# Kernel tuning notes

Hardware: AMD Instinct MI355X
Metric: run time of the kernel (lower is better)

The kernel has to match this reference:

```python
import jax, jax.numpy as jnp
import numpy as np


def setup_inputs() -> dict:
    key = jax.random.key(0)
    ks = jax.random.split(key, 10)
    B, T = 256, 256
    num_q, dk, dv, C = 1000, 128, 128, 32
    xn_k = (2.0 / (dk + C)) ** 0.5   # xavier_normal for Mk
    xn_v = (2.0 / (C + dv)) ** 0.5   # xavier_normal for Mv
    return dict(
        skills=jax.random.randint(ks[0], (B, T), 0, num_q),
        responses=jax.random.randint(ks[1], (B, T), 0, 2),
        k_emb=jax.random.normal(ks[2], (num_q, dk), dtype=jnp.float32) * 0.05,
        v_emb=jax.random.normal(ks[3], (2 * num_q, dv), dtype=jnp.float32) * 0.05,
        Mk=jax.random.normal(ks[4], (dk, C), dtype=jnp.float32) * xn_k,
        Mv0=jax.random.normal(ks[5], (C, dv), dtype=jnp.float32) * xn_v,
        f_W=jax.random.normal(ks[6], (2 * dk, dk), dtype=jnp.float32) * 0.05,
        f_b=jnp.zeros((dk,), jnp.float32),
        p_W=jax.random.normal(ks[7], (dk, 1), dtype=jnp.float32) * 0.05,
        p_b=jnp.zeros((1,), jnp.float32),
        e_W=jax.random.normal(ks[8], (dv, dv), dtype=jnp.float32) * 0.05,
        e_b=jnp.zeros((dv,), jnp.float32),
        a_W=jax.random.normal(ks[9], (dv, dv), dtype=jnp.float32) * 0.05,
        a_b=jnp.zeros((dv,), jnp.float32),
    )


def reference(skills, responses, k_emb, v_emb, Mk, Mv0, f_W, f_b,
              p_W, p_b, e_W, e_b, a_W, a_b):
    num_q = k_emb.shape[0]
    B = skills.shape[0]
    masked_r = responses * (responses > -1).astype(responses.dtype)
    qr = skills + num_q * masked_r
    kt_all = k_emb[skills]   # (B, T, dk)
    vt_all = v_emb[qr]       # (B, T, dv)
    Mvt0 = jnp.broadcast_to(Mv0[None], (B,) + Mv0.shape)  # (B, C, dv)

    def step(Mvt, xs):
        kt, vt = xs                                      # (B,dk), (B,dv)
        wt = jax.nn.softmax(kt @ Mk, axis=-1)            # (B, C) read weights
        rt = jnp.einsum('bc,bcd->bd', wt, Mvt)           # memory read
        ft = jnp.tanh(jnp.concatenate([rt, kt], axis=-1) @ f_W + f_b)
        pt = jax.nn.sigmoid(ft @ p_W + p_b)[:, 0]        # (B,)
        et = jax.nn.sigmoid(vt @ e_W + e_b)              # erase gate
        at = jnp.tanh(vt @ a_W + a_b)                    # add vector
        Mvt = Mvt * (1.0 - wt[:, :, None] * et[:, None, :]) \
              + wt[:, :, None] * at[:, None, :]
        return Mvt, pt

    xs = (jnp.swapaxes(kt_all, 0, 1), jnp.swapaxes(vt_all, 0, 1))  # time-major
    _, p = jax.lax.scan(step, Mvt0, xs)                  # (T, B)
    p = jnp.swapaxes(p, 0, 1)                            # (B, T)
    pred = p[:, :-1]
    true = responses[:, 1:].astype(jnp.float32)
    return pred, true
```

## Files before the change

kernel.cpp:

```cpp
#include <hip/hip_runtime.h>
#include <math.h>

#define BB 256
#define TT 256
#define NQ 1000
#define DK 128
#define DV 128
#define CC 32

typedef short s16x8 __attribute__((ext_vector_type(8)));
typedef float f32x4 __attribute__((ext_vector_type(4)));
typedef float f32x2 __attribute__((ext_vector_type(2)));

__device__ __forceinline__ float fast_sigmoid(float x) {
    x = fminf(fmaxf(x, -30.f), 30.f);
    return 1.f / (1.f + __expf(-x));
}
__device__ __forceinline__ float fast_tanh(float x) {
    x = fminf(fmaxf(x, -15.f), 15.f);
    float t = __expf(2.f * x);
    return (t - 1.f) / (t + 1.f);
}
__device__ __forceinline__ unsigned short f2bf(float f) {
    unsigned u = __float_as_uint(f);
    u += 0x7fffu + ((u >> 16) & 1u);
    return (unsigned short)(u >> 16);
}
__device__ __forceinline__ float bf2f(unsigned short h) {
    return __uint_as_float((unsigned)h << 16);
}
__device__ __forceinline__ unsigned u4get(uint4 v, int i) {
    return i == 0 ? v.x : i == 1 ? v.y : i == 2 ? v.z : v.w;
}
__device__ __forceinline__ f32x2 mk2(float x, float y) { f32x2 r; r.x = x; r.y = y; return r; }
__device__ __forceinline__ f32x2 fma2(f32x2 a, f32x2 b, f32x2 c) {
    return __builtin_elementwise_fma(a, b, c);
}
__device__ __forceinline__ s16x8 cvt8(float4 v0, float4 v1) {
    s16x8 f;
    f[0] = (short)f2bf(v0.x); f[1] = (short)f2bf(v0.y);
    f[2] = (short)f2bf(v0.z); f[3] = (short)f2bf(v0.w);
    f[4] = (short)f2bf(v1.x); f[5] = (short)f2bf(v1.y);
    f[6] = (short)f2bf(v1.z); f[7] = (short)f2bf(v1.w);
    return f;
}

__global__ __launch_bounds__(256) void conv_kernel(
    const float* __restrict__ eW, const float* __restrict__ aW,
    const float* __restrict__ fW, const float* __restrict__ Mk,
    unsigned short* __restrict__ eWt, unsigned short* __restrict__ aWt,
    unsigned short* __restrict__ fWat, unsigned short* __restrict__ fWbt,
    unsigned short* __restrict__ Mkt)
{
    int idx = blockIdx.x * 256 + threadIdx.x;
    if (idx < 16384) {
        int n = idx >> 7, k = idx & 127;
        eWt[idx] = f2bf(eW[k * 128 + n]);
    } else if (idx < 32768) {
        int i = idx - 16384; int n = i >> 7, k = i & 127;
        aWt[i] = f2bf(aW[k * 128 + n]);
    } else if (idx < 49152) {
        int i = idx - 32768; int n = i >> 7, k = i & 127;
        fWat[i] = f2bf(fW[k * 128 + n]);
    } else if (idx < 65536) {
        int i = idx - 49152; int n = i >> 7, k = i & 127;
        fWbt[i] = f2bf(fW[(128 + k) * 128 + n]);
    } else if (idx < 69632) {
        int i = idx - 65536; int n = i >> 7, k = i & 127;
        Mkt[i] = f2bf(Mk[k * 32 + n]);
    }
}

__global__ __launch_bounds__(256) void pre_kernel(
    const int* __restrict__ skills, const int* __restrict__ responses,
    const float* __restrict__ k_emb, const float* __restrict__ v_emb,
    const float* __restrict__ fb, const float* __restrict__ eb,
    const float* __restrict__ ab,
    const unsigned short* __restrict__ Mkt, const unsigned short* __restrict__ fWbt,
    const unsigned short* __restrict__ eWt, const unsigned short* __restrict__ aWt,
    float* __restrict__ Wo, unsigned* __restrict__ EA,
    unsigned short* __restrict__ Ko, float* __restrict__ outTrue,
    int t0, int Tc)
{
    const int tid = threadIdx.x;
    const int lane = tid & 63;
    const int m_base = (tid >> 6) * 16;
    const int mrow = lane & 15, quad = lane >> 4;
    const size_t base = (size_t)blockIdx.x * 64;

    __shared__ __align__(16) unsigned short Wlds[128 * 136];

    int grow = (int)base + m_base + mrow;
    int gb = grow / Tc;
    int gt = t0 + (grow - gb * Tc);
    int gi = gb * TT + gt;
    int s = skills[gi];
    int r = responses[gi];
    int q = s + NQ * ((r > -1) ? r : 0);
    if (quad == 0 && gt >= 1) outTrue[gb * (TT - 1) + (gt - 1)] = (float)r;

    {
        int n = tid >> 3, k0 = (tid & 7) * 16;
        *(s16x8*)&Wlds[n * 136 + k0]     = *(const s16x8*)&Mkt[n * 128 + k0];
        *(s16x8*)&Wlds[n * 136 + k0 + 8] = *(const s16x8*)&Mkt[n * 128 + k0 + 8];
    }

    s16x8 aF[4];
    {
        const float* kr = k_emb + (size_t)s * DK + quad * 8;
#pragma unroll
        for (int kb = 0; kb < 4; ++kb)
            aF[kb] = cvt8(*(const float4*)(kr + kb * 32),
                          *(const float4*)(kr + kb * 32 + 4));
    }
    __syncthreads();

    {
        f32x4 l0 = {0.f, 0.f, 0.f, 0.f}, l1 = {0.f, 0.f, 0.f, 0.f};
#pragma unroll
        for (int kb = 0; kb < 4; ++kb) {
            s16x8 b0 = *(const s16x8*)&Wlds[mrow * 136 + kb * 32 + quad * 8];
            s16x8 b1 = *(const s16x8*)&Wlds[(16 + mrow) * 136 + kb * 32 + quad * 8];
            l0 = __builtin_amdgcn_mfma_f32_16x16x32_bf16(aF[kb], b0, l0, 0, 0, 0);
            l1 = __builtin_amdgcn_mfma_f32_16x16x32_bf16(aF[kb], b1, l1, 0, 0, 0);
        }
#pragma unroll
        for (int reg = 0; reg < 4; ++reg) {
            float a0 = l0[reg], a1 = l1[reg];
            float m = fmaxf(a0, a1);
#pragma unroll
            for (int off = 1; off < 16; off <<= 1)
                m = fmaxf(m, __shfl_xor(m, off, 64));
            float e0 = __expf(a0 - m), e1 = __expf(a1 - m);
            float ssum = e0 + e1;
#pragma unroll
            for (int off = 1; off < 16; off <<= 1)
                ssum += __shfl_xor(ssum, off, 64);
            float inv = 1.f / ssum;
            size_t rowg = base + m_base + quad * 4 + reg;
            Wo[rowg * 32 + mrow]      = e0 * inv;
            Wo[rowg * 32 + 16 + mrow] = e1 * inv;
        }
    }
    __syncthreads();

    {
        int n = tid >> 1, k0 = (tid & 1) * 64;
#pragma unroll
        for (int j = 0; j < 8; ++j)
            *(s16x8*)&Wlds[n * 136 + k0 + j * 8] = *(const s16x8*)&fWbt[n * 128 + k0 + j * 8];
    }
    __syncthreads();

    s16x8 vF[4];
    {
        const float* vr = v_emb + (size_t)q * DV + quad * 8;
#pragma unroll
        for (int kb = 0; kb < 4; ++kb)
            vF[kb] = cvt8(*(const float4*)(vr + kb * 32),
                          *(const float4*)(vr + kb * 32 + 4));
    }

#pragma unroll
    for (int nt = 0; nt < 8; ++nt) {
        f32x4 acc = {0.f, 0.f, 0.f, 0.f};
#pragma unroll
        for (int kb = 0; kb < 4; ++kb) {
            s16x8 bf = *(const s16x8*)&Wlds[(nt * 16 + mrow) * 136 + kb * 32 + quad * 8];
            acc = __builtin_amdgcn_mfma_f32_16x16x32_bf16(aF[kb], bf, acc, 0, 0, 0);
        }
        int col = nt * 16 + mrow;
        float fbv = fb[col];
#pragma unroll
        for (int reg = 0; reg < 4; ++reg) {
            size_t rr = base + m_base + quad * 4 + reg;
            Ko[rr * 128 + col] = f2bf(acc[reg] + fbv);
        }
    }
    __syncthreads();

    {
        int n = tid >> 1, k0 = (tid & 1) * 64;
#pragma unroll
        for (int j = 0; j < 8; ++j)
            *(s16x8*)&Wlds[n * 136 + k0 + j * 8] = *(const s16x8*)&eWt[n * 128 + k0 + j * 8];
    }
    __syncthreads();

    float etr[8][4];
#pragma unroll
    for (int nt = 0; nt < 8; ++nt) {
        f32x4 acc = {0.f, 0.f, 0.f, 0.f};
#pragma unroll
        for (int kb = 0; kb < 4; ++kb) {
            s16x8 bf = *(const s16x8*)&Wlds[(nt * 16 + mrow) * 136 + kb * 32 + quad * 8];
            acc = __builtin_amdgcn_mfma_f32_16x16x32_bf16(vF[kb], bf, acc, 0, 0, 0);
        }
        int col = nt * 16 + mrow;
        float ebv = eb[col];
#pragma unroll
        for (int reg = 0; reg < 4; ++reg)
            etr[nt][reg] = fast_sigmoid(acc[reg] + ebv);
    }
    __syncthreads();

    {
        int n = tid >> 1, k0 = (tid & 1) * 64;
#pragma unroll
        for (int j = 0; j < 8; ++j)
            *(s16x8*)&Wlds[n * 136 + k0 + j * 8] = *(const s16x8*)&aWt[n * 128 + k0 + j * 8];
    }
    __syncthreads();

#pragma unroll
    for (int nt = 0; nt < 8; ++nt) {
        f32x4 acc = {0.f, 0.f, 0.f, 0.f};
#pragma unroll
        for (int kb = 0; kb < 4; ++kb) {
            s16x8 bf = *(const s16x8*)&Wlds[(nt * 16 + mrow) * 136 + kb * 32 + quad * 8];
            acc = __builtin_amdgcn_mfma_f32_16x16x32_bf16(vF[kb], bf, acc, 0, 0, 0);
        }
        int col = nt * 16 + mrow;
        float abv = ab[col];
#pragma unroll
        for (int reg = 0; reg < 4; ++reg) {
            size_t rr = base + m_base + quad * 4 + reg;
            int bb = (int)(rr / (size_t)Tc);
            int t  = (int)(rr - (size_t)bb * Tc);
            size_t o4 = (((size_t)bb * (Tc >> 5) + (t >> 5)) * 8 + ((t >> 2) & 7)) * 128 + col;
            unsigned lo = f2bf(etr[nt][reg]);
            unsigned hi = (unsigned)f2bf(fast_tanh(acc[reg] + abv)) << 16;
            EA[o4 * 4 + (t & 3)] = hi | lo;
        }
    }
}


#define CH 32
#define WROW 36
#define RSTR 136
#define SB() __builtin_amdgcn_sched_barrier(0)

#define LOAD_W(gg) do {                                                       \
    const float* ws = Wb + (size_t)(gg) * CH * 32;                            \
    wr0 = *(const float4*)(ws + tid * 8);                                     \
    wr1 = *(const float4*)(ws + tid * 8 + 4);                                 \
} while (0)

#define PUB_W(gg) do {                                                        \
    float* wd = &Wl[(gg) & 1][lr * WROW + lq * 8];                            \
    *(float4*)wd = wr0; *(float4*)(wd + 4) = wr1;                             \
} while (0)

#define LOAD_EA(ER, gg) do {                                                  \
    const uint4* src = EA4 + ((size_t)(bq + (gg))) * 1024 + tid;              \
    _Pragma("unroll")                                                         \
    for (int j = 0; j < 8; ++j) ER[j] = src[j * 128];                         \
} while (0)

#define PREF8(A0,A1,A2,A3,A4,A5,A6,A7, rowidx) do {                           \
    const float* _wr = wlc + (rowidx) * WROW;                                 \
    A0 = *(const float4*)(_wr + 0);  A1 = *(const float4*)(_wr + 4);          \
    A2 = *(const float4*)(_wr + 8);  A3 = *(const float4*)(_wr + 12);         \
    A4 = *(const float4*)(_wr + 16); A5 = *(const float4*)(_wr + 20);         \
    A6 = *(const float4*)(_wr + 24); A7 = *(const float4*)(_wr + 28);         \
} while (0)

#define STEP8(A0,A1,A2,A3,A4,A5,A6,A7, ER, tl) do {                           \
    f32x2 w2[16];                                                             \
    w2[0]  = mk2(A0.x, A0.y); w2[1]  = mk2(A0.z, A0.w);                       \
    w2[2]  = mk2(A1.x, A1.y); w2[3]  = mk2(A1.z, A1.w);                       \
    w2[4]  = mk2(A2.x, A2.y); w2[5]  = mk2(A2.z, A2.w);                       \
    w2[6]  = mk2(A3.x, A3.y); w2[7]  = mk2(A3.z, A3.w);                       \
    w2[8]  = mk2(A4.x, A4.y); w2[9]  = mk2(A4.z, A4.w);                       \
    w2[10] = mk2(A5.x, A5.y); w2[11] = mk2(A5.z, A5.w);                       \
    w2[12] = mk2(A6.x, A6.y); w2[13] = mk2(A6.z, A6.w);                       \
    w2[14] = mk2(A7.x, A7.y); w2[15] = mk2(A7.z, A7.w);                       \
    unsigned ea = u4get(ER[(tl) >> 2], (tl) & 3);                             \
    float e = __uint_as_float(ea << 16);                                      \
    float a = __uint_as_float(ea & 0xffff0000u);                              \
    f32x2 ne2 = mk2(-e, -e);                                                  \
    f32x2 a2  = mk2(a, a);                                                    \
    f32x2 r0 = mk2(0.f, 0.f), r1 = r0, r2 = r0, r3 = r0;                      \
    _Pragma("unroll")                                                         \
    for (int q = 0; q < 4; ++q) {                                             \
        r0 = fma2(w2[4*q+0], Mv2[4*q+0], r0);                                 \
        r1 = fma2(w2[4*q+1], Mv2[4*q+1], r1);                                 \
        r2 = fma2(w2[4*q+2], Mv2[4*q+2], r2);                                 \
        r3 = fma2(w2[4*q+3], Mv2[4*q+3], r3);                                 \
    }                                                                         \
    f32x2 rs = (r0 + r1) + (r2 + r3);                                         \
    slp[(tl) * RSTR + tid] = f2bf(rs.x + rs.y);                               \
    _Pragma("unroll")                                                         \
    for (int i = 0; i < 16; ++i)                                              \
        Mv2[i] = fma2(w2[i], fma2(ne2, Mv2[i], a2), Mv2[i]);                  \
} while (0)

#define SEQ_CHUNK(ER, gg, SL) do {                                            \
    const float* wlc = Wl[(gg) & 1];                                          \
    unsigned short* slp = SL;                                                 \
    PREF8(w0,w1,w2_,w3_,w4_,w5_,w6_,w7_, 0);                                  \
    _Pragma("unroll")                                                         \
    for (int tp = 0; tp < 16; ++tp) {                                         \
        SB(); PREF8(u0,u1,u2,u3,u4,u5,u6,u7, 2 * tp + 1); SB();               \
        STEP8(w0,w1,w2_,w3_,w4_,w5_,w6_,w7_, ER, 2 * tp);                     \
        SB(); PREF8(w0,w1,w2_,w3_,w4_,w5_,w6_,w7_,                            \
                    (2 * tp + 2 < 32) ? (2 * tp + 2) : 31); SB();             \
        STEP8(u0,u1,u2,u3,u4,u5,u6,u7, ER, 2 * tp + 1);                       \
    }                                                                         \
} while (0)

__device__ __forceinline__ void consume_chunk(
    int gc, const unsigned short* sl, const unsigned short* fWl,
    int b, int Tc, int t0,
    const unsigned short* __restrict__ Ko, const float* __restrict__ pW,
    float pbv, float* __restrict__ pred, int tid)
{
    const int lane = tid & 63;
    const int cw = (tid >> 6) & 1;
    const int mrow = lane & 15, quad = lane >> 4;
    s16x8 aF[4];
#pragma unroll
    for (int kb = 0; kb < 4; ++kb)
        aF[kb] = *(const s16x8*)&sl[(cw * 16 + mrow) * RSTR + kb * 32 + quad * 8];
    float p0 = 0.f, p1 = 0.f, p2 = 0.f, p3 = 0.f;
    size_t rbase = (size_t)b * Tc + gc * CH + cw * 16 + quad * 4;
#pragma unroll
    for (int nt = 0; nt < 8; ++nt) {
        f32x4 acc = {0.f, 0.f, 0.f, 0.f};
#pragma unroll
        for (int kb = 0; kb < 4; ++kb) {
            s16x8 bf = *(const s16x8*)&fWl[(nt * 16 + mrow) * RSTR + kb * 32 + quad * 8];
            acc = __builtin_amdgcn_mfma_f32_16x16x32_bf16(aF[kb], bf, acc, 0, 0, 0);
        }
        int col = nt * 16 + mrow;
        float pw = pW[col];
        p0 = fmaf(fast_tanh(acc[0] + bf2f(Ko[(rbase + 0) * 128 + col])), pw, p0);
        p1 = fmaf(fast_tanh(acc[1] + bf2f(Ko[(rbase + 1) * 128 + col])), pw, p1);
        p2 = fmaf(fast_tanh(acc[2] + bf2f(Ko[(rbase + 2) * 128 + col])), pw, p2);
        p3 = fmaf(fast_tanh(acc[3] + bf2f(Ko[(rbase + 3) * 128 + col])), pw, p3);
    }
#pragma unroll
    for (int off = 1; off < 16; off <<= 1) {
        p0 += __shfl_xor(p0, off, 64); p1 += __shfl_xor(p1, off, 64);
        p2 += __shfl_xor(p2, off, 64); p3 += __shfl_xor(p3, off, 64);
    }
    if (mrow == 0) {
        int tb = t0 + gc * CH + cw * 16 + quad * 4;
        float ps[4] = {p0, p1, p2, p3};
#pragma unroll
        for (int reg = 0; reg < 4; ++reg) {
            int t = tb + reg;
            if (t < TT - 1) pred[b * (TT - 1) + t] = fast_sigmoid(ps[reg] + pbv);
        }
    }
}

__global__ __launch_bounds__(256, 1) void fused_kernel(
    const float* __restrict__ W, const unsigned* __restrict__ EA,
    const float* __restrict__ Mv0, const unsigned short* __restrict__ Ko,
    const unsigned short* __restrict__ fWat, const float* __restrict__ pW,
    const float* __restrict__ pb,
    float* __restrict__ pred, float* __restrict__ MvWS,
    int t0, int Tc, int doInit, int doSave)
{
    const int b = blockIdx.x;
    const int tid = threadIdx.x;
    const int nch = Tc / CH;

    __shared__ __align__(16) float Wl[2][CH * WROW];
    __shared__ __align__(16) unsigned short rtl[2][CH * RSTR];
    __shared__ __align__(16) unsigned short fWl[128 * RSTR];

    {
        int n = tid >> 1, k0 = (tid & 1) * 64;
#pragma unroll
        for (int j = 0; j < 8; ++j)
            *(s16x8*)&fWl[n * RSTR + k0 + j * 8] = *(const s16x8*)&fWat[n * 128 + k0 + j * 8];
    }

    const int lr = tid >> 2, lq = tid & 3;
    const float* __restrict__ Wb = W + (size_t)b * Tc * 32;
    const uint4* __restrict__ EA4 = (const uint4*)EA;
    const int bq = b * nch;
    f32x2 Mv2[16];
    float4 wr0, wr1;
    float4 w0, w1, w2_, w3_, w4_, w5_, w6_, w7_;
    float4 u0, u1, u2, u3, u4, u5, u6, u7;
    uint4 erA[8], erB[8];
    float pbv = 0.f;

    if (tid < 128) {
        if (doInit) {
#pragma unroll
            for (int i = 0; i < 16; ++i)
                Mv2[i] = mk2(Mv0[(2 * i) * 128 + tid], Mv0[(2 * i + 1) * 128 + tid]);
        } else {
#pragma unroll
            for (int i = 0; i < 16; ++i)
                Mv2[i] = mk2(MvWS[(size_t)b * 4096 + (2 * i) * 128 + tid],
                             MvWS[(size_t)b * 4096 + (2 * i + 1) * 128 + tid]);
        }
        LOAD_W(0); PUB_W(0);
        LOAD_EA(erA, 0);
        if (nch > 1) LOAD_W(1);
    } else {
        pbv = pb[0];
    }
    __syncthreads();

    for (int g = 0; g < nch; g += 2) {
        if (tid < 128) {
            if (g + 1 < nch) PUB_W(g + 1);
            if (g + 2 < nch) LOAD_W(g + 2);
            if (g + 1 < nch) LOAD_EA(erB, g + 1);
            SEQ_CHUNK(erA, g, rtl[0]);
        } else if (g >= 1) {
            consume_chunk(g - 1, rtl[1], fWl, b, Tc, t0, Ko, pW, pbv, pred, tid);
        }
        __syncthreads();

        if (tid < 128) {
            if (g + 1 < nch) {
                if (g + 2 < nch) PUB_W(g + 2);
                if (g + 3 < nch) LOAD_W(g + 3);
                if (g + 2 < nch) LOAD_EA(erA, g + 2);
                SEQ_CHUNK(erB, g + 1, rtl[1]);
            }
        } else {
            consume_chunk(g, rtl[0], fWl, b, Tc, t0, Ko, pW, pbv, pred, tid);
        }
        __syncthreads();
    }
    if (!(nch & 1) && tid >= 128) {
        consume_chunk(nch - 1, rtl[1], fWl, b, Tc, t0, Ko, pW, pbv, pred, tid);
    }

    if (doSave && tid < 128) {
#pragma unroll
        for (int i = 0; i < 16; ++i) {
            MvWS[(size_t)b * 4096 + (2 * i) * 128 + tid]     = Mv2[i].x;
            MvWS[(size_t)b * 4096 + (2 * i + 1) * 128 + tid] = Mv2[i].y;
        }
    }
}


extern "C" void kernel_launch(void* const* d_in, const int* in_sizes, int n_in,
                              void* d_out, int out_size, void* d_ws, size_t ws_size,
                              hipStream_t stream) {
    const int*   skills    = (const int*)d_in[0];
    const int*   responses = (const int*)d_in[1];
    const float* k_emb     = (const float*)d_in[2];
    const float* v_emb     = (const float*)d_in[3];
    const float* Mk        = (const float*)d_in[4];
    const float* Mv0       = (const float*)d_in[5];
    const float* f_W       = (const float*)d_in[6];
    const float* f_b       = (const float*)d_in[7];
    const float* p_W       = (const float*)d_in[8];
    const float* p_b       = (const float*)d_in[9];
    const float* e_W       = (const float*)d_in[10];
    const float* e_b       = (const float*)d_in[11];
    const float* a_W       = (const float*)d_in[12];
    const float* a_b       = (const float*)d_in[13];

    float* pred    = (float*)d_out;
    float* outTrue = pred + BB * (TT - 1);

    int Tc = TT;
    for (;;) {
        size_t need = (size_t)BB * Tc * 896 + 69632 * 2;
        if (Tc < TT) need += (size_t)BB * 4096 * 4;
        if (need <= ws_size || Tc <= 32) break;
        Tc >>= 1;
    }

    char* p = (char*)d_ws;
    float* Wo = (float*)p;                     p += (size_t)BB * Tc * 32 * 4;
    unsigned* EA = (unsigned*)p;               p += (size_t)BB * Tc * 128 * 4;
    unsigned short* Ko = (unsigned short*)p;   p += (size_t)BB * Tc * 128 * 2;
    unsigned short* eWt = (unsigned short*)p;  p += 16384 * 2;
    unsigned short* aWt = (unsigned short*)p;  p += 16384 * 2;
    unsigned short* fWat = (unsigned short*)p; p += 16384 * 2;
    unsigned short* fWbt = (unsigned short*)p; p += 16384 * 2;
    unsigned short* Mkt = (unsigned short*)p;  p += 4096 * 2;
    float* MvWS = (float*)p;

    conv_kernel<<<272, 256, 0, stream>>>(e_W, a_W, f_W, Mk,
                                         eWt, aWt, fWat, fWbt, Mkt);

    for (int t0 = 0; t0 < TT; t0 += Tc) {
        pre_kernel<<<(BB * Tc) / 64, 256, 0, stream>>>(
            skills, responses, k_emb, v_emb, f_b, e_b, a_b,
            Mkt, fWbt, eWt, aWt, Wo, EA, Ko, outTrue, t0, Tc);
        fused_kernel<<<BB, 256, 0, stream>>>(
            Wo, EA, Mv0, Ko, fWat, p_W, p_b, pred, MvWS,
            t0, Tc, t0 == 0 ? 1 : 0, (t0 + Tc < TT) ? 1 : 0);
    }
}
```

Measured before the change: 165.3 us.

## Load per-step read weights via scalar loads instead of LDS staging

The softmax read weights for each step are now fetched directly into scalar registers with s_load_dwordx16, double-buffered across steps, replacing the global-to-LDS publish and per-step LDS vector reads. The consumer warps prefetch the whole batch row's weights into cache at kernel start so the scalar loads hit cache. The producer/consumer split uses a wave-uniform flag. This removes LDS traffic and VGPR pressure from the serial recurrence, at the cost of scalar-cache latency on the critical path and one extra global read pass. One scalar load is issued past the end of each chunk, and the last step reads beyond the row's weights.

```diff
diff --git a/kernel.cpp b/kernel.cpp
--- a/kernel.cpp
+++ b/kernel.cpp
@@ -11,6 +11,7 @@
 typedef short s16x8 __attribute__((ext_vector_type(8)));
 typedef float f32x4 __attribute__((ext_vector_type(4)));
 typedef float f32x2 __attribute__((ext_vector_type(2)));
+typedef float f32x16 __attribute__((ext_vector_type(16)));
 
 __device__ __forceinline__ float fast_sigmoid(float x) {
     x = fminf(fmaxf(x, -30.f), 30.f);
@@ -237,20 +238,7 @@
 
 
 #define CH 32
-#define WROW 36
 #define RSTR 136
-#define SB() __builtin_amdgcn_sched_barrier(0)
-
-#define LOAD_W(gg) do {                                                       \
-    const float* ws = Wb + (size_t)(gg) * CH * 32;                            \
-    wr0 = *(const float4*)(ws + tid * 8);                                     \
-    wr1 = *(const float4*)(ws + tid * 8 + 4);                                 \
-} while (0)
-
-#define PUB_W(gg) do {                                                        \
-    float* wd = &Wl[(gg) & 1][lr * WROW + lq * 8];                            \
-    *(float4*)wd = wr0; *(float4*)(wd + 4) = wr1;                             \
-} while (0)
 
 #define LOAD_EA(ER, gg) do {                                                  \
     const uint4* src = EA4 + ((size_t)(bq + (gg))) * 1024 + tid;              \
@@ -258,55 +246,56 @@
     for (int j = 0; j < 8; ++j) ER[j] = src[j * 128];                         \
 } while (0)
 
-#define PREF8(A0,A1,A2,A3,A4,A5,A6,A7, rowidx) do {                           \
-    const float* _wr = wlc + (rowidx) * WROW;                                 \
-    A0 = *(const float4*)(_wr + 0);  A1 = *(const float4*)(_wr + 4);          \
-    A2 = *(const float4*)(_wr + 8);  A3 = *(const float4*)(_wr + 12);         \
-    A4 = *(const float4*)(_wr + 16); A5 = *(const float4*)(_wr + 20);         \
-    A6 = *(const float4*)(_wr + 24); A7 = *(const float4*)(_wr + 28);         \
+#define WLOAD(B0, B1, gs) do {                                                \
+    unsigned long long _up = (unsigned long long)(Wb + (size_t)(gs) * 32);    \
+    unsigned _lo = __builtin_amdgcn_readfirstlane((unsigned)_up);             \
+    unsigned _hi = __builtin_amdgcn_readfirstlane((unsigned)(_up >> 32));     \
+    unsigned long long _sp = ((unsigned long long)_hi << 32) | _lo;           \
+    asm volatile("s_load_dwordx16 %0, %2, 0\n\t"                              \
+                 "s_load_dwordx16 %1, %2, 64"                                 \
+                 : "=s"(B0), "=s"(B1) : "s"(_sp));                            \
 } while (0)
 
-#define STEP8(A0,A1,A2,A3,A4,A5,A6,A7, ER, tl) do {                           \
-    f32x2 w2[16];                                                             \
-    w2[0]  = mk2(A0.x, A0.y); w2[1]  = mk2(A0.z, A0.w);                       \
-    w2[2]  = mk2(A1.x, A1.y); w2[3]  = mk2(A1.z, A1.w);                       \
-    w2[4]  = mk2(A2.x, A2.y); w2[5]  = mk2(A2.z, A2.w);                       \
-    w2[6]  = mk2(A3.x, A3.y); w2[7]  = mk2(A3.z, A3.w);                       \
-    w2[8]  = mk2(A4.x, A4.y); w2[9]  = mk2(A4.z, A4.w);                       \
-    w2[10] = mk2(A5.x, A5.y); w2[11] = mk2(A5.z, A5.w);                       \
-    w2[12] = mk2(A6.x, A6.y); w2[13] = mk2(A6.z, A6.w);                       \
-    w2[14] = mk2(A7.x, A7.y); w2[15] = mk2(A7.z, A7.w);                       \
+#define WWAIT(B0, B1)                                                         \
+    asm volatile("s_waitcnt lgkmcnt(0)" : "+s"(B0), "+s"(B1))
+
+#define WOP(WL, J, MVI, ACC) do {                                             \
+    f32x2 wp = __builtin_shufflevector(WL, WL, 2 * (J), 2 * (J) + 1);         \
+    ACC = fma2(wp, Mv2[MVI], ACC);                                            \
+    f32x2 t1 = fma2(ne2, Mv2[MVI], a2);                                       \
+    Mv2[MVI] = fma2(wp, t1, Mv2[MVI]);                                        \
+} while (0)
+
+#define STEPW(WL0, WL1, ER, tl) do {                                          \
     unsigned ea = u4get(ER[(tl) >> 2], (tl) & 3);                             \
-    float e = __uint_as_float(ea << 16);                                      \
-    float a = __uint_as_float(ea & 0xffff0000u);                              \
+    float e  = __uint_as_float(ea << 16);                                     \
+    float av = __uint_as_float(ea & 0xffff0000u);                             \
     f32x2 ne2 = mk2(-e, -e);                                                  \
-    f32x2 a2  = mk2(a, a);                                                    \
-    f32x2 r0 = mk2(0.f, 0.f), r1 = r0, r2 = r0, r3 = r0;                      \
-    _Pragma("unroll")                                                         \
-    for (int q = 0; q < 4; ++q) {                                             \
-        r0 = fma2(w2[4*q+0], Mv2[4*q+0], r0);                                 \
-        r1 = fma2(w2[4*q+1], Mv2[4*q+1], r1);                                 \
-        r2 = fma2(w2[4*q+2], Mv2[4*q+2], r2);                                 \
-        r3 = fma2(w2[4*q+3], Mv2[4*q+3], r3);                                 \
-    }                                                                         \
-    f32x2 rs = (r0 + r1) + (r2 + r3);                                         \
+    f32x2 a2  = mk2(av, av);                                                  \
+    f32x2 racc0 = mk2(0.f, 0.f), racc1 = racc0, racc2 = racc0, racc3 = racc0; \
+    WOP(WL0, 0, 0, racc0);  WOP(WL0, 1, 1, racc1);                            \
+    WOP(WL0, 2, 2, racc2);  WOP(WL0, 3, 3, racc3);                            \
+    WOP(WL0, 4, 4, racc0);  WOP(WL0, 5, 5, racc1);                            \
+    WOP(WL0, 6, 6, racc2);  WOP(WL0, 7, 7, racc3);                            \
+    WOP(WL1, 0, 8, racc0);  WOP(WL1, 1, 9, racc1);                            \
+    WOP(WL1, 2, 10, racc2); WOP(WL1, 3, 11, racc3);                           \
+    WOP(WL1, 4, 12, racc0); WOP(WL1, 5, 13, racc1);                           \
+    WOP(WL1, 6, 14, racc2); WOP(WL1, 7, 15, racc3);                           \
+    f32x2 rs = (racc0 + racc1) + (racc2 + racc3);                             \
     slp[(tl) * RSTR + tid] = f2bf(rs.x + rs.y);                               \
-    _Pragma("unroll")                                                         \
-    for (int i = 0; i < 16; ++i)                                              \
-        Mv2[i] = fma2(w2[i], fma2(ne2, Mv2[i], a2), Mv2[i]);                  \
 } while (0)
 
-#define SEQ_CHUNK(ER, gg, SL) do {                                            \
-    const float* wlc = Wl[(gg) & 1];                                          \
+#define SEQ_CHUNKW(ER, gg, SL) do {                                           \
     unsigned short* slp = SL;                                                 \
-    PREF8(w0,w1,w2_,w3_,w4_,w5_,w6_,w7_, 0);                                  \
     _Pragma("unroll")                                                         \
     for (int tp = 0; tp < 16; ++tp) {                                         \
-        SB(); PREF8(u0,u1,u2,u3,u4,u5,u6,u7, 2 * tp + 1); SB();               \
-        STEP8(w0,w1,w2_,w3_,w4_,w5_,w6_,w7_, ER, 2 * tp);                     \
-        SB(); PREF8(w0,w1,w2_,w3_,w4_,w5_,w6_,w7_,                            \
-                    (2 * tp + 2 < 32) ? (2 * tp + 2) : 31); SB();             \
-        STEP8(u0,u1,u2,u3,u4,u5,u6,u7, ER, 2 * tp + 1);                       \
+        int gs = (gg) * 32 + 2 * tp;                                          \
+        WWAIT(wA0, wA1);                                                      \
+        WLOAD(wB0, wB1, gs + 1);                                              \
+        STEPW(wA0, wA1, ER, 2 * tp);                                          \
+        WWAIT(wB0, wB1);                                                      \
+        WLOAD(wA0, wA1, gs + 2);                                              \
+        STEPW(wB0, wB1, ER, 2 * tp + 1);                                      \
     }                                                                         \
 } while (0)
 
@@ -367,8 +356,8 @@
     const int b = blockIdx.x;
     const int tid = threadIdx.x;
     const int nch = Tc / CH;
-
-    __shared__ __align__(16) float Wl[2][CH * WROW];
+    const int prod = (__builtin_amdgcn_readfirstlane(tid) >> 7) == 0;
+
     __shared__ __align__(16) unsigned short rtl[2][CH * RSTR];
     __shared__ __align__(16) unsigned short fWl[128 * RSTR];
 
@@ -379,18 +368,15 @@
             *(s16x8*)&fWl[n * RSTR + k0 + j * 8] = *(const s16x8*)&fWat[n * 128 + k0 + j * 8];
     }
 
-    const int lr = tid >> 2, lq = tid & 3;
     const float* __restrict__ Wb = W + (size_t)b * Tc * 32;
     const uint4* __restrict__ EA4 = (const uint4*)EA;
     const int bq = b * nch;
     f32x2 Mv2[16];
-    float4 wr0, wr1;
-    float4 w0, w1, w2_, w3_, w4_, w5_, w6_, w7_;
-    float4 u0, u1, u2, u3, u4, u5, u6, u7;
+    f32x16 wA0, wA1, wB0, wB1;
     uint4 erA[8], erB[8];
     float pbv = 0.f;
 
-    if (tid < 128) {
+    if (prod) {
         if (doInit) {
 #pragma unroll
             for (int i = 0; i < 16; ++i)
@@ -401,42 +387,44 @@
                 Mv2[i] = mk2(MvWS[(size_t)b * 4096 + (2 * i) * 128 + tid],
                              MvWS[(size_t)b * 4096 + (2 * i + 1) * 128 + tid]);
         }
-        LOAD_W(0); PUB_W(0);
+        WLOAD(wA0, wA1, 0);
         LOAD_EA(erA, 0);
-        if (nch > 1) LOAD_W(1);
     } else {
         pbv = pb[0];
+        const float4* Wt4 = (const float4*)Wb;
+        int j = tid - 128;
+#pragma unroll 4
+        for (; j < Tc * 8; j += 128) {
+            float4 tch = Wt4[j];
+            asm volatile("" :: "v"(tch.x), "v"(tch.y), "v"(tch.z), "v"(tch.w));
+        }
     }
     __syncthreads();
 
     for (int g = 0; g < nch; g += 2) {
-        if (tid < 128) {
-            if (g + 1 < nch) PUB_W(g + 1);
-            if (g + 2 < nch) LOAD_W(g + 2);
+        if (prod) {
             if (g + 1 < nch) LOAD_EA(erB, g + 1);
-            SEQ_CHUNK(erA, g, rtl[0]);
+            SEQ_CHUNKW(erA, g, rtl[0]);
         } else if (g >= 1) {
             consume_chunk(g - 1, rtl[1], fWl, b, Tc, t0, Ko, pW, pbv, pred, tid);
         }
         __syncthreads();
 
-        if (tid < 128) {
+        if (prod) {
             if (g + 1 < nch) {
-                if (g + 2 < nch) PUB_W(g + 2);
-                if (g + 3 < nch) LOAD_W(g + 3);
                 if (g + 2 < nch) LOAD_EA(erA, g + 2);
-                SEQ_CHUNK(erB, g + 1, rtl[1]);
+                SEQ_CHUNKW(erB, g + 1, rtl[1]);
             }
         } else {
             consume_chunk(g, rtl[0], fWl, b, Tc, t0, Ko, pW, pbv, pred, tid);
         }
         __syncthreads();
     }
-    if (!(nch & 1) && tid >= 128) {
+    if (!(nch & 1) && !prod) {
         consume_chunk(nch - 1, rtl[1], fWl, b, Tc, t0, Ko, pW, pbv, pred, tid);
     }
 
-    if (doSave && tid < 128) {
+    if (doSave && prod) {
 #pragma unroll
         for (int i = 0; i < 16; ++i) {
             MvWS[(size_t)b * 4096 + (2 * i) * 128 + tid]     = Mv2[i].x;
```

After: 209.8 us. 26.9% more time.

## Split memory-slot recurrence across all 256 threads and serialize consume after each chunk

Applied to the files above, without the earlier changes.

The sequential memory update is now spread over all 256 threads, with each thread holding 16 of the 32 memory slots for one value column. Partial read sums are combined with a lane shuffle. This halves the per-thread serial FMA chain and register load, but it drops the previous producer/consumer overlap: instead of 128 threads running the recurrence while the other 128 did the MFMA consume, every chunk now runs the recurrence, then a barrier, then the consume. The serial critical path is shorter, but consume time is no longer hidden.

```diff
diff --git a/kernel.cpp b/kernel.cpp
--- a/kernel.cpp
+++ b/kernel.cpp
@@ -243,70 +243,64 @@
 
 #define LOAD_W(gg) do {                                                       \
     const float* ws = Wb + (size_t)(gg) * CH * 32;                            \
-    wr0 = *(const float4*)(ws + tid * 8);                                     \
-    wr1 = *(const float4*)(ws + tid * 8 + 4);                                 \
-} while (0)
-
-#define PUB_W(gg) do {                                                        \
-    float* wd = &Wl[(gg) & 1][lr * WROW + lq * 8];                            \
+    int t2 = tid & 127;                                                       \
+    wr0 = *(const float4*)(ws + t2 * 8);                                      \
+    wr1 = *(const float4*)(ws + t2 * 8 + 4);                                  \
+} while (0)
+
+#define PUB_W() do {                                                          \
+    float* wd = &Wl[lr * WROW + lq * 8];                                      \
     *(float4*)wd = wr0; *(float4*)(wd + 4) = wr1;                             \
 } while (0)
 
 #define LOAD_EA(ER, gg) do {                                                  \
-    const uint4* src = EA4 + ((size_t)(bq + (gg))) * 1024 + tid;              \
+    const uint4* src = EA4 + ((size_t)(bq + (gg))) * 1024 + dd;               \
     _Pragma("unroll")                                                         \
     for (int j = 0; j < 8; ++j) ER[j] = src[j * 128];                         \
 } while (0)
 
-#define PREF8(A0,A1,A2,A3,A4,A5,A6,A7, rowidx) do {                           \
+#define PREF4(A0,A1,A2,A3, rowidx) do {                                       \
     const float* _wr = wlc + (rowidx) * WROW;                                 \
     A0 = *(const float4*)(_wr + 0);  A1 = *(const float4*)(_wr + 4);          \
     A2 = *(const float4*)(_wr + 8);  A3 = *(const float4*)(_wr + 12);         \
-    A4 = *(const float4*)(_wr + 16); A5 = *(const float4*)(_wr + 20);         \
-    A6 = *(const float4*)(_wr + 24); A7 = *(const float4*)(_wr + 28);         \
-} while (0)
-
-#define STEP8(A0,A1,A2,A3,A4,A5,A6,A7, ER, tl) do {                           \
-    f32x2 w2[16];                                                             \
-    w2[0]  = mk2(A0.x, A0.y); w2[1]  = mk2(A0.z, A0.w);                       \
-    w2[2]  = mk2(A1.x, A1.y); w2[3]  = mk2(A1.z, A1.w);                       \
-    w2[4]  = mk2(A2.x, A2.y); w2[5]  = mk2(A2.z, A2.w);                       \
-    w2[6]  = mk2(A3.x, A3.y); w2[7]  = mk2(A3.z, A3.w);                       \
-    w2[8]  = mk2(A4.x, A4.y); w2[9]  = mk2(A4.z, A4.w);                       \
-    w2[10] = mk2(A5.x, A5.y); w2[11] = mk2(A5.z, A5.w);                       \
-    w2[12] = mk2(A6.x, A6.y); w2[13] = mk2(A6.z, A6.w);                       \
-    w2[14] = mk2(A7.x, A7.y); w2[15] = mk2(A7.z, A7.w);                       \
+} while (0)
+
+#define STEP4(A0,A1,A2,A3, ER, tl) do {                                       \
+    f32x2 w2[8];                                                              \
+    w2[0] = mk2(A0.x, A0.y); w2[1] = mk2(A0.z, A0.w);                         \
+    w2[2] = mk2(A1.x, A1.y); w2[3] = mk2(A1.z, A1.w);                         \
+    w2[4] = mk2(A2.x, A2.y); w2[5] = mk2(A2.z, A2.w);                         \
+    w2[6] = mk2(A3.x, A3.y); w2[7] = mk2(A3.z, A3.w);                         \
     unsigned ea = u4get(ER[(tl) >> 2], (tl) & 3);                             \
-    float e = __uint_as_float(ea << 16);                                      \
-    float a = __uint_as_float(ea & 0xffff0000u);                              \
+    float e  = __uint_as_float(ea << 16);                                     \
+    float av = __uint_as_float(ea & 0xffff0000u);                             \
     f32x2 ne2 = mk2(-e, -e);                                                  \
-    f32x2 a2  = mk2(a, a);                                                    \
+    f32x2 a2  = mk2(av, av);                                                  \
     f32x2 r0 = mk2(0.f, 0.f), r1 = r0, r2 = r0, r3 = r0;                      \
+    r0 = fma2(w2[0], Mv2[0], r0); r1 = fma2(w2[1], Mv2[1], r1);               \
+    r2 = fma2(w2[2], Mv2[2], r2); r3 = fma2(w2[3], Mv2[3], r3);               \
+    r0 = fma2(w2[4], Mv2[4], r0); r1 = fma2(w2[5], Mv2[5], r1);               \
+    r2 = fma2(w2[6], Mv2[6], r2); r3 = fma2(w2[7], Mv2[7], r3);               \
+    f32x2 rs = (r0 + r1) + (r2 + r3);                                         \
+    float sum = rs.x + rs.y;                                                  \
+    sum += __shfl_xor(sum, 1, 64);                                            \
+    slp[(tl) * RSTR + dd] = f2bf(sum);    \
     _Pragma("unroll")                                                         \
-    for (int q = 0; q < 4; ++q) {                                             \
-        r0 = fma2(w2[4*q+0], Mv2[4*q+0], r0);                                 \
-        r1 = fma2(w2[4*q+1], Mv2[4*q+1], r1);                                 \
-        r2 = fma2(w2[4*q+2], Mv2[4*q+2], r2);                                 \
-        r3 = fma2(w2[4*q+3], Mv2[4*q+3], r3);                                 \
-    }                                                                         \
-    f32x2 rs = (r0 + r1) + (r2 + r3);                                         \
-    slp[(tl) * RSTR + tid] = f2bf(rs.x + rs.y);                               \
-    _Pragma("unroll")                                                         \
-    for (int i = 0; i < 16; ++i)                                              \
+    for (int i = 0; i < 8; ++i)                                               \
         Mv2[i] = fma2(w2[i], fma2(ne2, Mv2[i], a2), Mv2[i]);                  \
 } while (0)
 
-#define SEQ_CHUNK(ER, gg, SL) do {                                            \
-    const float* wlc = Wl[(gg) & 1];                                          \
+#define SEQ_CHUNK4(ER, gg, SL) do {                                           \
+    const float* wlc = Wl + hh * 16;                                          \
     unsigned short* slp = SL;                                                 \
-    PREF8(w0,w1,w2_,w3_,w4_,w5_,w6_,w7_, 0);                                  \
+    PREF4(w0, w1, w2_, w3_, 0);                                               \
     _Pragma("unroll")                                                         \
     for (int tp = 0; tp < 16; ++tp) {                                         \
-        SB(); PREF8(u0,u1,u2,u3,u4,u5,u6,u7, 2 * tp + 1); SB();               \
-        STEP8(w0,w1,w2_,w3_,w4_,w5_,w6_,w7_, ER, 2 * tp);                     \
-        SB(); PREF8(w0,w1,w2_,w3_,w4_,w5_,w6_,w7_,                            \
+        SB(); PREF4(u0, u1, u2, u3, 2 * tp + 1); SB();                        \
+        STEP4(w0, w1, w2_, w3_, ER, 2 * tp);                                  \
+        SB(); PREF4(w0, w1, w2_, w3_,                                         \
                     (2 * tp + 2 < 32) ? (2 * tp + 2) : 31); SB();             \
-        STEP8(u0,u1,u2,u3,u4,u5,u6,u7, ER, 2 * tp + 1);                       \
+        STEP4(u0, u1, u2, u3, ER, 2 * tp + 1);                                \
     }                                                                         \
 } while (0)
 
@@ -367,9 +361,11 @@
     const int b = blockIdx.x;
     const int tid = threadIdx.x;
     const int nch = Tc / CH;
-
-    __shared__ __align__(16) float Wl[2][CH * WROW];
-    __shared__ __align__(16) unsigned short rtl[2][CH * RSTR];
+    const int dd = tid >> 1;
+    const int hh = tid & 1;
+
+    __shared__ __align__(16) float Wl[CH * WROW];
+    __shared__ __align__(16) unsigned short rtl[CH * RSTR];
     __shared__ __align__(16) unsigned short fWl[128 * RSTR];
 
     {
@@ -379,68 +375,55 @@
             *(s16x8*)&fWl[n * RSTR + k0 + j * 8] = *(const s16x8*)&fWat[n * 128 + k0 + j * 8];
     }
 
-    const int lr = tid >> 2, lq = tid & 3;
+    const int lr = (tid & 127) >> 2, lq = tid & 3;
     const float* __restrict__ Wb = W + (size_t)b * Tc * 32;
     const uint4* __restrict__ EA4 = (const uint4*)EA;
     const int bq = b * nch;
-    f32x2 Mv2[16];
+    f32x2 Mv2[8];
     float4 wr0, wr1;
-    float4 w0, w1, w2_, w3_, w4_, w5_, w6_, w7_;
-    float4 u0, u1, u2, u3, u4, u5, u6, u7;
-    uint4 erA[8], erB[8];
-    float pbv = 0.f;
-
-    if (tid < 128) {
-        if (doInit) {
-#pragma unroll
-            for (int i = 0; i < 16; ++i)
-                Mv2[i] = mk2(Mv0[(2 * i) * 128 + tid], Mv0[(2 * i + 1) * 128 + tid]);
-        } else {
-#pragma unroll
-            for (int i = 0; i < 16; ++i)
-                Mv2[i] = mk2(MvWS[(size_t)b * 4096 + (2 * i) * 128 + tid],
-                             MvWS[(size_t)b * 4096 + (2 * i + 1) * 128 + tid]);
-        }
-        LOAD_W(0); PUB_W(0);
-        LOAD_EA(erA, 0);
+    float4 w0, w1, w2_, w3_;
+    float4 u0, u1, u2, u3;
+    uint4 erA[8];
+    float pbv = pb[0];
+
+    if (tid >= 128) LOAD_W(0);
+
+    if (doInit) {
+#pragma unroll
+        for (int i = 0; i < 8; ++i)
+            Mv2[i] = mk2(Mv0[(hh * 16 + 2 * i) * 128 + dd],
+                         Mv0[(hh * 16 + 2 * i + 1) * 128 + dd]);
+    } else {
+#pragma unroll
+        for (int i = 0; i < 8; ++i)
+            Mv2[i] = mk2(MvWS[(size_t)b * 4096 + (hh * 16 + 2 * i) * 128 + dd],
+                         MvWS[(size_t)b * 4096 + (hh * 16 + 2 * i + 1) * 128 + dd]);
+    }
+    LOAD_EA(erA, 0);
+    if (tid >= 128) {
+        PUB_W();
         if (nch > 1) LOAD_W(1);
-    } else {
-        pbv = pb[0];
-    }
-    __syncthreads();
-
-    for (int g = 0; g < nch; g += 2) {
+    }
+    __syncthreads();
+
+    for (int g = 0; g < nch; ++g) {
+        SEQ_CHUNK4(erA, g, rtl);
+        __syncthreads();
+        if (g + 1 < nch) LOAD_EA(erA, g + 1);
         if (tid < 128) {
-            if (g + 1 < nch) PUB_W(g + 1);
+            consume_chunk(g, rtl, fWl, b, Tc, t0, Ko, pW, pbv, pred, tid);
+        } else if (g + 1 < nch) {
+            PUB_W();
             if (g + 2 < nch) LOAD_W(g + 2);
-            if (g + 1 < nch) LOAD_EA(erB, g + 1);
-            SEQ_CHUNK(erA, g, rtl[0]);
-        } else if (g >= 1) {
-            consume_chunk(g - 1, rtl[1], fWl, b, Tc, t0, Ko, pW, pbv, pred, tid);
         }
         __syncthreads();
-
-        if (tid < 128) {
-            if (g + 1 < nch) {
-                if (g + 2 < nch) PUB_W(g + 2);
-                if (g + 3 < nch) LOAD_W(g + 3);
-                if (g + 2 < nch) LOAD_EA(erA, g + 2);
-                SEQ_CHUNK(erB, g + 1, rtl[1]);
-            }
-        } else {
-            consume_chunk(g, rtl[0], fWl, b, Tc, t0, Ko, pW, pbv, pred, tid);
-        }
-        __syncthreads();
-    }
-    if (!(nch & 1) && tid >= 128) {
-        consume_chunk(nch - 1, rtl[1], fWl, b, Tc, t0, Ko, pW, pbv, pred, tid);
-    }
-
-    if (doSave && tid < 128) {
-#pragma unroll
-        for (int i = 0; i < 16; ++i) {
-            MvWS[(size_t)b * 4096 + (2 * i) * 128 + tid]     = Mv2[i].x;
-            MvWS[(size_t)b * 4096 + (2 * i + 1) * 128 + tid] = Mv2[i].y;
+    }
+
+    if (doSave) {
+#pragma unroll
+        for (int i = 0; i < 8; ++i) {
+            MvWS[(size_t)b * 4096 + (hh * 16 + 2 * i) * 128 + dd]     = Mv2[i].x;
+            MvWS[(size_t)b * 4096 + (hh * 16 + 2 * i + 1) * 128 + dd] = Mv2[i].y;
         }
     }
 }
```

New measurement: 202.3 us. 1.22x slower.
